# Kernel optimization log

Measured on AMD Instinct MI355X. Metric: run time of the kernel, lower is better.

Reference implementation:

```python
import jax, jax.numpy as jnp
import numpy as np

NUM_ACTIONS = 16  # number of unique leaf actions (= output_dim)


def setup_inputs() -> dict:
    key = jax.random.key(0)
    ks = jax.random.split(key, 7)
    B, IN, D, A = 32768, 128, 511, 512
    L = D + A + 1  # 1024 leaves
    x = jax.random.normal(ks[0], (B, IN), dtype=jnp.float32)
    Wd = jax.random.normal(ks[1], (D, IN), dtype=jnp.float32) * 0.05
    bd = jax.random.normal(ks[2], (D,), dtype=jnp.float32) * 0.05
    Wa = jax.random.normal(ks[3], (A, IN), dtype=jnp.float32) * 0.05
    ba = jax.random.normal(ks[4], (A,), dtype=jnp.float32) * 0.05
    Wl = jax.random.normal(ks[5], (L, 2 * (D + A)), dtype=jnp.float32) * 0.05
    seg_ids = jax.random.randint(ks[6], (L,), 0, NUM_ACTIONS, dtype=jnp.int32)
    return {"x": x, "Wd": Wd, "bd": bd, "Wa": Wa, "ba": ba, "Wl": Wl,
            "seg_ids": seg_ids}


def reference(x, Wd, bd, Wa, ba, Wl, seg_ids):
    # dual linear heads (torch Linear: y = x @ W.T + b)
    x1 = x @ Wd.T + bd            # [B, D]
    x2 = x @ Wa.T + ba            # [B, A]
    h = jnp.concatenate([x1, x2], axis=1)                     # [B, D+A]
    hh = jnp.concatenate([jax.nn.relu(h), jax.nn.relu(-h)], axis=1)  # [B, 2(D+A)]
    leaf = hh @ Wl.T              # [B, L]
    # ragged per-action max over leaf columns (MaxPoolLayer)
    pooled = jax.ops.segment_max(leaf.T, seg_ids,
                                 num_segments=NUM_ACTIONS).T   # [B, NUM_ACTIONS]
    return jax.nn.softmax(pooled, axis=-1)
```

## Files before the change

### kernel.cpp

```cpp
#include <hip/hip_runtime.h>
#include <hip/hip_bf16.h>
#include <cstdint>
#include <cmath>

#define AS1 __attribute__((address_space(1)))
#define AS3 __attribute__((address_space(3)))

typedef unsigned short u16;
typedef uint32_t u32;
typedef __attribute__((ext_vector_type(8))) __bf16 bf16x8;
typedef __attribute__((ext_vector_type(8))) unsigned short u16x8;
typedef __attribute__((ext_vector_type(4))) float f32x4;


__device__ __forceinline__ u16 f2bf(float f) {
    uint32_t u = __builtin_bit_cast(uint32_t, f);
    return (u16)((u + 0x7fffu + ((u >> 16) & 1u)) >> 16);
}

__device__ __forceinline__ u32 f2ord(float f) {
    u32 u = __builtin_bit_cast(u32, f);
    return u ^ (u32)(((int32_t)u >> 31) | 0x80000000);
}
__device__ __forceinline__ float ord2f(u32 v) {
    u32 u = (v & 0x80000000u) ? (v ^ 0x80000000u) : ~v;
    return __builtin_bit_cast(float, u);
}


__global__ void setup_all(const float* __restrict__ x,
                          const float* __restrict__ Wd, const float* __restrict__ bd,
                          const float* __restrict__ Wa, const float* __restrict__ ba,
                          const float* __restrict__ Wl,
                          u16* __restrict__ xb, u16* __restrict__ w1b,
                          float* __restrict__ bb, u16* __restrict__ w1t,
                          u16* __restrict__ wsb, u16* __restrict__ dlb,
                          float* __restrict__ cl, u32* __restrict__ pooled) {
    __shared__ float cred[256];
    const int b = blockIdx.x;
    const int tid = threadIdx.x;
    if (b < 2048) {
        long idx = (long)(b * 256 + tid) * 8;
        float4 a = *(const float4*)(x + idx);
        float4 c = *(const float4*)(x + idx + 4);
        u16x8 o;
        o[0]=f2bf(a.x); o[1]=f2bf(a.y); o[2]=f2bf(a.z); o[3]=f2bf(a.w);
        o[4]=f2bf(c.x); o[5]=f2bf(c.y); o[6]=f2bf(c.z); o[7]=f2bf(c.w);
        *(u16x8*)(xb + idx) = o;
    } else if (b < 2112) {
        int t = (b - 2048) * 256 + tid;
        int row = t >> 4, g = (t & 15) * 8;
        const float* src = nullptr;
        if (row < 511)       src = Wd + row * 128 + g;
        else if (row < 1023) src = Wa + (row - 511) * 128 + g;
        u16x8 o = 0;
        if (src) {
            #pragma unroll
            for (int j = 0; j < 8; ++j) o[j] = f2bf(src[j]);
        }
        *(u16x8*)(w1b + row * 128 + g) = o;
        #pragma unroll
        for (int j = 0; j < 8; ++j) w1t[(g + j) * 1024 + row] = o[j];
        if ((t & 15) == 0)
            bb[row] = row < 511 ? bd[row] : (row < 1023 ? ba[row - 511] : 0.f);
    } else if (b < 2624) {
        const int l0 = (b - 2112) * 2;
        const int lo = tid >> 7, g = (tid & 127) * 8;
        const float* src = Wl + (long)(l0 + lo) * 2046;
        u16x8 os, od;
        float part = 0.f;
        #pragma unroll
        for (int j = 0; j < 8; ++j) {
            int c = g + j;
            float pa = 0.f, pb = 0.f;
            if (c < 1023) { pa = src[c]; pb = src[1023 + c]; }
            os[j] = f2bf(0.5f * (pa + pb));
            float v = pa - pb;
            od[j] = f2bf(v);
            float b1 = c < 511 ? bd[c] : (c < 1023 ? ba[c - 511] : 0.f);
            part += v * b1;
        }
        *(u16x8*)(wsb + (long)(l0 + lo) * 1024 + g) = os;
        *(u16x8*)(dlb + (long)(l0 + lo) * 1024 + g) = od;
        cred[tid] = part;
        __syncthreads();
        if (tid < 2) {
            float s = 0.f;
            #pragma unroll
            for (int k = 0; k < 128; ++k) s += cred[tid * 128 + k];
            cl[l0 + tid] = 0.5f * s;
        }
    } else {
        uint4* p4 = (uint4*)pooled;
        const int base = (b - 2624) * 16384;
        #pragma unroll
        for (int j = 0; j < 64; ++j)
            p4[base + tid + j * 256] = uint4{0u, 0u, 0u, 0u};
    }
}

__global__ __launch_bounds__(256) void gemm_hwc(
        const u16* __restrict__ xb, const u16* __restrict__ w1b,
        const float* __restrict__ bb,
        const u16* __restrict__ dlb, const u16* __restrict__ w1t,
        u16* __restrict__ habs, u16* __restrict__ wcb) {
    __shared__ union SharedU {
        struct { u16 As[2][4096]; u16 Bs[2][4096]; } s;
        u16 obuf[128 * 132];
    } sh;
    const int tid  = threadIdx.x;
    const int lane = tid & 63, wave = tid >> 6;
    const int wy = wave >> 1, wx = wave & 1;
    const int i16 = lane & 15, q = lane >> 4;
    const int cA = wave * 2, srow = lane >> 2;
    const int scol = (((lane & 3) ^ ((lane >> 3) & 3))) * 8;
    const int qa   = (q ^ ((i16 >> 1) & 3)) * 8;

    f32x4 acc[4][4];
    #pragma unroll
    for (int m = 0; m < 4; ++m)
        #pragma unroll
        for (int n = 0; n < 4; ++n) acc[m][n] = f32x4{0.f,0.f,0.f,0.f};

    if (blockIdx.y == 0) {
        const long blockM = (long)blockIdx.x * 128;
        const int koff = (blockIdx.x * 4) & 31;
        const u16* a0 = dlb + (blockM + cA * 16 + srow) * 1024 + scol;
        const u16* a1 = dlb + (blockM + (cA + 1) * 16 + srow) * 1024 + scol;
        const u16* b0 = w1t + (long)(cA * 16 + srow) * 1024 + scol;
        const u16* b1 = w1t + (long)((cA + 1) * 16 + srow) * 1024 + scol;
        auto wstage = [&](int tt) {
            const int sl = tt & 1;
            const int k0 = ((tt + koff) & 31) << 5;
            __builtin_amdgcn_global_load_lds((const AS1 void*)(a0 + k0), (AS3 void*)&sh.s.As[sl][cA * 512],       16, 0, 0);
            __builtin_amdgcn_global_load_lds((const AS1 void*)(a1 + k0), (AS3 void*)&sh.s.As[sl][(cA + 1) * 512], 16, 0, 0);
            __builtin_amdgcn_global_load_lds((const AS1 void*)(b0 + k0), (AS3 void*)&sh.s.Bs[sl][cA * 512],       16, 0, 0);
            __builtin_amdgcn_global_load_lds((const AS1 void*)(b1 + k0), (AS3 void*)&sh.s.Bs[sl][(cA + 1) * 512], 16, 0, 0);
        };
        wstage(0);
        asm volatile("s_waitcnt vmcnt(0)" ::: "memory");
        __builtin_amdgcn_s_barrier();
        for (int t = 0; t < 32; ++t) {
            const int sl = t & 1;
            __builtin_amdgcn_sched_barrier(0);
            bf16x8 af[4], bfv[4];
            #pragma unroll
            for (int s = 0; s < 4; ++s) {
                af[s]  = *(const bf16x8*)&sh.s.As[sl][(wy * 64 + s * 16 + i16) * 32 + qa];
                bfv[s] = *(const bf16x8*)&sh.s.Bs[sl][(wx * 64 + s * 16 + i16) * 32 + qa];
            }
            if (t + 1 < 32) wstage(t + 1);
            asm volatile("s_waitcnt lgkmcnt(0)" ::: "memory");
            __builtin_amdgcn_sched_barrier(0);
            __builtin_amdgcn_s_setprio(1);
            #pragma unroll
            for (int sm = 0; sm < 4; ++sm)
                #pragma unroll
                for (int sn = 0; sn < 4; ++sn)
                    acc[sm][sn] = __builtin_amdgcn_mfma_f32_16x16x32_bf16(af[sm], bfv[sn], acc[sm][sn], 0, 0, 0);
            __builtin_amdgcn_s_setprio(0);
            if (t + 1 < 32) { asm volatile("s_waitcnt vmcnt(0)" ::: "memory"); }
            __builtin_amdgcn_s_barrier();
        }
        #pragma unroll
        for (int sm = 0; sm < 4; ++sm)
            #pragma unroll
            for (int sn = 0; sn < 4; ++sn) {
                const int col = wx * 64 + sn * 16 + i16;
                #pragma unroll
                for (int r = 0; r < 4; ++r) {
                    const long row = blockM + wy * 64 + sm * 16 + 4 * q + r;
                    wcb[row * 128 + col] = f2bf(0.5f * acc[sm][sn][r]);
                }
            }
        return;
    }

    const int xcd = blockIdx.x, yy = blockIdx.y - 1;
    const long blockM = (long)(xcd * 32 + (yy >> 3)) * 128;
    const int  blockN = (yy & 7) * 128;

    const u16* a0 = xb + (blockM + cA * 16 + srow) * 128 + scol;
    const u16* a1 = xb + (blockM + (cA + 1) * 16 + srow) * 128 + scol;
    const u16* b0 = w1b + ((long)blockN + cA * 16 + srow) * 128 + scol;
    const u16* b1 = w1b + ((long)blockN + (cA + 1) * 16 + srow) * 128 + scol;
    auto hstage = [&](int tt) {
        const int sl = tt & 1, kp = tt * 32;
        __builtin_amdgcn_global_load_lds((const AS1 void*)(a0 + kp), (AS3 void*)&sh.s.As[sl][cA * 512],       16, 0, 0);
        __builtin_amdgcn_global_load_lds((const AS1 void*)(a1 + kp), (AS3 void*)&sh.s.As[sl][(cA + 1) * 512], 16, 0, 0);
        __builtin_amdgcn_global_load_lds((const AS1 void*)(b0 + kp), (AS3 void*)&sh.s.Bs[sl][cA * 512],       16, 0, 0);
        __builtin_amdgcn_global_load_lds((const AS1 void*)(b1 + kp), (AS3 void*)&sh.s.Bs[sl][(cA + 1) * 512], 16, 0, 0);
    };
    hstage(0);
    asm volatile("s_waitcnt vmcnt(0)" ::: "memory");
    __builtin_amdgcn_s_barrier();
    #pragma unroll
    for (int kt = 0; kt < 4; ++kt) {
        const int sl = kt & 1;
        __builtin_amdgcn_sched_barrier(0);
        bf16x8 af[4], bfv[4];
        #pragma unroll
        for (int s = 0; s < 4; ++s) {
            af[s]  = *(const bf16x8*)&sh.s.As[sl][(wy * 64 + s * 16 + i16) * 32 + qa];
            bfv[s] = *(const bf16x8*)&sh.s.Bs[sl][(wx * 64 + s * 16 + i16) * 32 + qa];
        }
        if (kt + 1 < 4) hstage(kt + 1);
        asm volatile("s_waitcnt lgkmcnt(0)" ::: "memory");
        __builtin_amdgcn_sched_barrier(0);
        __builtin_amdgcn_s_setprio(1);
        #pragma unroll
        for (int sm = 0; sm < 4; ++sm)
            #pragma unroll
            for (int sn = 0; sn < 4; ++sn)
                acc[sm][sn] = __builtin_amdgcn_mfma_f32_16x16x32_bf16(af[sm], bfv[sn], acc[sm][sn], 0, 0, 0);
        __builtin_amdgcn_s_setprio(0);
        if (kt + 1 < 4) { asm volatile("s_waitcnt vmcnt(0)" ::: "memory"); }
        __builtin_amdgcn_s_barrier();
    }

    float bv[4];
    #pragma unroll
    for (int sn = 0; sn < 4; ++sn) bv[sn] = bb[blockN + wx * 64 + sn * 16 + i16];
    #pragma unroll
    for (int sm = 0; sm < 4; ++sm)
        #pragma unroll
        for (int sn = 0; sn < 4; ++sn)
            #pragma unroll
            for (int r = 0; r < 4; ++r)
                sh.obuf[(wy * 64 + sm * 16 + 4 * q + r) * 132 + wx * 64 + sn * 16 + i16] =
                    f2bf(fabsf(acc[sm][sn][r] + bv[sn]));
    __syncthreads();
    const int cg = (tid & 15) * 8;
    #pragma unroll
    for (int it = 0; it < 8; ++it) {
        const int row = it * 16 + (tid >> 4);
        *(u16x8*)&habs[(blockM + row) * 1024 + blockN + cg] =
            *(const u16x8*)&sh.obuf[row * 132 + cg];
    }
}

__global__ __launch_bounds__(512, 2) void gemm_leaf(const u16* __restrict__ habs,
        const u16* __restrict__ xb, const u16* __restrict__ wsb,
        const u16* __restrict__ wcb, const float* __restrict__ cl,
        const int* __restrict__ seg, u32* __restrict__ pooled) {
    __shared__ __align__(16) u16 As[4][256 * 32];
    __shared__ __align__(16) u16 Bs[4][256 * 32];
    __shared__ u32 pmax[256 * 16];
    const int tid  = threadIdx.x;
    const int lane = tid & 63, w = tid >> 6;
    const int wm = w >> 2, wn = w & 3;
    const int i16 = lane & 15, q = lane >> 4;

    const int bid  = blockIdx.x;
    const int wgid = (bid & 7) * 64 + (bid >> 3);
    const int mT = wgid >> 2, nT = wgid & 3;
    const long blockM = (long)mT * 256;
    const int  blockN = nT * 256;

    #pragma unroll
    for (int j = 0; j < 8; ++j) pmax[tid + j * 512] = 0u;

    const int r0 = tid >> 2;
    const int scol = (((tid & 3) ^ ((tid >> 3) & 3))) * 8;
    const u16* gA1 = habs + (blockM + r0) * 1024 + scol;
    const u16* gB1 = wsb  + (long)(blockN + r0) * 1024 + scol;
    const u16* gA2 = xb   + (blockM + r0) * 128 + scol;
    const u16* gB2 = wcb  + (long)(blockN + r0) * 128 + scol;
    const int ldsb = w * 512;

    auto stageA = [&](int tt) {
        u16* dst = &As[tt & 3][ldsb];
        const u16* g; int jstr;
        if (tt < 32) { g = gA1 + tt * 32;        jstr = 128 * 1024; }
        else         { g = gA2 + (tt - 32) * 32; jstr = 128 * 128; }
        __builtin_amdgcn_global_load_lds((const AS1 void*)g,          (AS3 void*)dst,          16, 0, 0);
        __builtin_amdgcn_global_load_lds((const AS1 void*)(g + jstr), (AS3 void*)(dst + 4096), 16, 0, 0);
    };
    auto stageB = [&](int tt) {
        u16* dst = &Bs[tt & 3][ldsb];
        const u16* g; int jstr;
        if (tt < 32) { g = gB1 + tt * 32;        jstr = 128 * 1024; }
        else         { g = gB2 + (tt - 32) * 32; jstr = 128 * 128; }
        __builtin_amdgcn_global_load_lds((const AS1 void*)g,          (AS3 void*)dst,          16, 0, 0);
        __builtin_amdgcn_global_load_lds((const AS1 void*)(g + jstr), (AS3 void*)(dst + 4096), 16, 0, 0);
    };

    f32x4 acc[8][4];
    #pragma unroll
    for (int m = 0; m < 8; ++m)
        #pragma unroll
        for (int n = 0; n < 4; ++n) acc[m][n] = f32x4{0.f,0.f,0.f,0.f};
    bf16x8 a0r[4], a1r[4], br[4];

    const int rdc = (q ^ ((i16 >> 1) & 3)) * 8;
    auto lda = [&](bf16x8* ar, int slot, int mh) {
        #pragma unroll
        for (int mf = 0; mf < 4; ++mf)
            ar[mf] = *(const bf16x8*)&As[slot][(wm * 128 + mh * 64 + mf * 16 + i16) * 32 + rdc];
    };
    auto ldb = [&](int slot) {
        #pragma unroll
        for (int nf = 0; nf < 4; ++nf)
            br[nf] = *(const bf16x8*)&Bs[slot][(wn * 64 + nf * 16 + i16) * 32 + rdc];
    };
    auto mf16 = [&](const bf16x8* ar, int mh) {
        #pragma unroll
        for (int mf = 0; mf < 4; ++mf)
            #pragma unroll
            for (int nf = 0; nf < 4; ++nf)
                acc[mh * 4 + mf][nf] = __builtin_amdgcn_mfma_f32_16x16x32_bf16(
                    ar[mf], br[nf], acc[mh * 4 + mf][nf], 0, 0, 0);
    };

    stageA(0); stageB(0); stageA(1); stageB(1);
    asm volatile("s_waitcnt vmcnt(4)" ::: "memory");
    __builtin_amdgcn_s_barrier();
    __builtin_amdgcn_sched_barrier(0);
    lda(a0r, 0, 0); ldb(0);

    for (int t = 0; t < 36; ++t) {
        const int slot = t & 3;
        lda(a1r, slot, 1);
        if (t + 2 < 36) { stageA(t + 2); stageB(t + 2); }
        asm volatile("s_waitcnt lgkmcnt(4)" ::: "memory");
        __builtin_amdgcn_sched_barrier(0);
        __builtin_amdgcn_s_setprio(1);
        mf16(a0r, 0);
        __builtin_amdgcn_s_setprio(0);
        asm volatile("s_waitcnt lgkmcnt(0)" ::: "memory");
        __builtin_amdgcn_sched_barrier(0);
        __builtin_amdgcn_s_setprio(1);
        mf16(a1r, 1);
        __builtin_amdgcn_s_setprio(0);
        if (t < 34)       { asm volatile("s_waitcnt vmcnt(4)" ::: "memory"); }
        else if (t == 34) { asm volatile("s_waitcnt vmcnt(0)" ::: "memory"); }
        __builtin_amdgcn_s_barrier();
        __builtin_amdgcn_sched_barrier(0);
        if (t + 1 < 36) { lda(a0r, (t + 1) & 3, 0); ldb((t + 1) & 3); }
    }

    int segc[4]; float clv[4];
    #pragma unroll
    for (int nf = 0; nf < 4; ++nf) {
        const int col = blockN + wn * 64 + nf * 16 + i16;
        segc[nf] = seg[col];
        clv[nf]  = cl[col];
    }
    #pragma unroll
    for (int mf = 0; mf < 8; ++mf)
        #pragma unroll
        for (int nf = 0; nf < 4; ++nf)
            #pragma unroll
            for (int r = 0; r < 4; ++r) {
                const int rl = wm * 128 + mf * 16 + 4 * q + r;
                atomicMax(&pmax[rl * 16 + segc[nf]], f2ord(acc[mf][nf][r] + clv[nf]));
            }
    __syncthreads();
    #pragma unroll
    for (int j = 0; j < 8; ++j) {
        int idx = tid + j * 512;
        atomicMax(&pooled[((blockM + (idx >> 4)) << 4) + (idx & 15)], pmax[idx]);
    }
}

__global__ __launch_bounds__(256) void finalize(const u32* __restrict__ pooled,
                                                float* __restrict__ out) {
    const int tid = threadIdx.x;
    const long row = (long)blockIdx.x * 16 + (tid >> 4);
    const int t = tid & 15;
    float logit = ord2f(pooled[(row << 4) + t]);
    float rm = logit;
    #pragma unroll
    for (int d = 8; d >= 1; d >>= 1) rm = fmaxf(rm, __shfl_xor(rm, d, 16));
    float e = __expf(logit - rm);
    float s = e;
    #pragma unroll
    for (int d = 8; d >= 1; d >>= 1) s += __shfl_xor(s, d, 16);
    out[(row << 4) + t] = e / s;
}

extern "C" void kernel_launch(void* const* d_in, const int* in_sizes, int n_in,
                              void* d_out, int out_size, void* d_ws, size_t ws_size,
                              hipStream_t stream) {
    const float* x  = (const float*)d_in[0];
    const float* Wd = (const float*)d_in[1];
    const float* bd = (const float*)d_in[2];
    const float* Wa = (const float*)d_in[3];
    const float* ba = (const float*)d_in[4];
    const float* Wl = (const float*)d_in[5];
    const int*  seg = (const int*)d_in[6];
    float* out = (float*)d_out;

    char* ws = (char*)d_ws;
    u16*   xb   = (u16*)(ws);
    u16*   w1b  = (u16*)(ws + 8388608);
    float* bb   = (float*)(ws + 8650752);
    u16*   w1t  = (u16*)(ws + 8654848);
    u16*   wsb  = (u16*)(ws + 8916992);
    u16*   dlb  = (u16*)(ws + 11014144);
    u16*   wcb  = (u16*)(ws + 13111296);
    float* clp  = (float*)(ws + 13373440);
    u16*   habs = (u16*)(ws + 13377536);
    u32*   pooled = (u32*)(ws + 80486400);

    setup_all<<<2632, 256, 0, stream>>>(x, Wd, bd, Wa, ba, Wl,
                                        xb, w1b, bb, w1t, wsb, dlb, clp, pooled);
    gemm_hwc <<<dim3(8, 257), 256, 0, stream>>>(xb, w1b, bb, dlb, w1t, habs, wcb);
    gemm_leaf<<<512, 512, 0, stream>>>(habs, xb, wsb, wcb, clp, seg, pooled);
    finalize <<<2048, 256, 0, stream>>>(pooled, out);
}
```

Baseline: 197.5 us.

## Shrink leaf GEMM tile to 128x256 with 4 waves and double-buffered LDS

The leaf GEMM moves from 256x256 tiles with 8 waves and a 4-stage LDS ring to 128x256 tiles with 4 waves (each wave computing 64x128) and a 2-stage buffer, launched as 1024 blocks instead of 512. The smaller per-block LDS footprint should let more blocks be resident and give finer load balancing across CUs. In exchange, B tiles are reloaded twice as often, arithmetic intensity per block is lower, and prefetch depth drops to one stage with a full vmcnt(0) wait every iteration, which exposes more memory latency.

```diff
diff --git a/kernel.cpp b/kernel.cpp
--- a/kernel.cpp
+++ b/kernel.cpp
@@ -239,26 +239,26 @@
     }
 }
 
-__global__ __launch_bounds__(512, 2) void gemm_leaf(const u16* __restrict__ habs,
+__global__ __launch_bounds__(256, 2) void gemm_leaf(const u16* __restrict__ habs,
         const u16* __restrict__ xb, const u16* __restrict__ wsb,
         const u16* __restrict__ wcb, const float* __restrict__ cl,
         const int* __restrict__ seg, u32* __restrict__ pooled) {
-    __shared__ __align__(16) u16 As[4][256 * 32];
-    __shared__ __align__(16) u16 Bs[4][256 * 32];
-    __shared__ u32 pmax[256 * 16];
+    __shared__ __align__(16) u16 As[2][128 * 32];
+    __shared__ __align__(16) u16 Bs[2][256 * 32];
+    __shared__ u32 pmax[128 * 16];
     const int tid  = threadIdx.x;
-    const int lane = tid & 63, w = tid >> 6;
-    const int wm = w >> 2, wn = w & 3;
+    const int lane = tid & 63, wave = tid >> 6;
+    const int wm = wave >> 1, wn = wave & 1;
     const int i16 = lane & 15, q = lane >> 4;
 
     const int bid  = blockIdx.x;
-    const int wgid = (bid & 7) * 64 + (bid >> 3);
+    const int wgid = (bid & 7) * 128 + (bid >> 3);
     const int mT = wgid >> 2, nT = wgid & 3;
-    const long blockM = (long)mT * 256;
+    const long blockM = (long)mT * 128;
     const int  blockN = nT * 256;
 
     #pragma unroll
-    for (int j = 0; j < 8; ++j) pmax[tid + j * 512] = 0u;
+    for (int j = 0; j < 8; ++j) pmax[tid + j * 256] = 0u;
 
     const int r0 = tid >> 2;
     const int scol = (((tid & 3) ^ ((tid >> 3) & 3))) * 8;
@@ -266,99 +266,100 @@
     const u16* gB1 = wsb  + (long)(blockN + r0) * 1024 + scol;
     const u16* gA2 = xb   + (blockM + r0) * 128 + scol;
     const u16* gB2 = wcb  + (long)(blockN + r0) * 128 + scol;
-    const int ldsb = w * 512;
+    const int ldsb = wave * 512;
 
     auto stageA = [&](int tt) {
-        u16* dst = &As[tt & 3][ldsb];
-        const u16* g; int jstr;
-        if (tt < 32) { g = gA1 + tt * 32;        jstr = 128 * 1024; }
-        else         { g = gA2 + (tt - 32) * 32; jstr = 128 * 128; }
+        u16* dst = &As[tt & 1][ldsb];
+        const u16* g; long jstr;
+        if (tt < 32) { g = gA1 + tt * 32;        jstr = 64L * 1024; }
+        else         { g = gA2 + (tt - 32) * 32; jstr = 64L * 128; }
         __builtin_amdgcn_global_load_lds((const AS1 void*)g,          (AS3 void*)dst,          16, 0, 0);
-        __builtin_amdgcn_global_load_lds((const AS1 void*)(g + jstr), (AS3 void*)(dst + 4096), 16, 0, 0);
+        __builtin_amdgcn_global_load_lds((const AS1 void*)(g + jstr), (AS3 void*)(dst + 2048), 16, 0, 0);
     };
     auto stageB = [&](int tt) {
-        u16* dst = &Bs[tt & 3][ldsb];
-        const u16* g; int jstr;
-        if (tt < 32) { g = gB1 + tt * 32;        jstr = 128 * 1024; }
-        else         { g = gB2 + (tt - 32) * 32; jstr = 128 * 128; }
-        __builtin_amdgcn_global_load_lds((const AS1 void*)g,          (AS3 void*)dst,          16, 0, 0);
-        __builtin_amdgcn_global_load_lds((const AS1 void*)(g + jstr), (AS3 void*)(dst + 4096), 16, 0, 0);
-    };
-
-    f32x4 acc[8][4];
-    #pragma unroll
-    for (int m = 0; m < 8; ++m)
-        #pragma unroll
-        for (int n = 0; n < 4; ++n) acc[m][n] = f32x4{0.f,0.f,0.f,0.f};
-    bf16x8 a0r[4], a1r[4], br[4];
+        u16* dst = &Bs[tt & 1][ldsb];
+        const u16* g; long jstr;
+        if (tt < 32) { g = gB1 + tt * 32;        jstr = 64L * 1024; }
+        else         { g = gB2 + (tt - 32) * 32; jstr = 64L * 128; }
+        #pragma unroll
+        for (int k = 0; k < 4; ++k)
+            __builtin_amdgcn_global_load_lds((const AS1 void*)(g + k * jstr),
+                                             (AS3 void*)(dst + k * 2048), 16, 0, 0);
+    };
+
+    f32x4 acc[4][8];
+    #pragma unroll
+    for (int m = 0; m < 4; ++m)
+        #pragma unroll
+        for (int n = 0; n < 8; ++n) acc[m][n] = f32x4{0.f,0.f,0.f,0.f};
+    bf16x8 a[4], b[8];
 
     const int rdc = (q ^ ((i16 >> 1) & 3)) * 8;
-    auto lda = [&](bf16x8* ar, int slot, int mh) {
+    auto lda = [&](int slot) {
         #pragma unroll
         for (int mf = 0; mf < 4; ++mf)
-            ar[mf] = *(const bf16x8*)&As[slot][(wm * 128 + mh * 64 + mf * 16 + i16) * 32 + rdc];
-    };
-    auto ldb = [&](int slot) {
+            a[mf] = *(const bf16x8*)&As[slot][(wm * 64 + mf * 16 + i16) * 32 + rdc];
+    };
+    auto ldbh = [&](int slot, int h) {
         #pragma unroll
         for (int nf = 0; nf < 4; ++nf)
-            br[nf] = *(const bf16x8*)&Bs[slot][(wn * 64 + nf * 16 + i16) * 32 + rdc];
-    };
-    auto mf16 = [&](const bf16x8* ar, int mh) {
+            b[h * 4 + nf] = *(const bf16x8*)&Bs[slot][(wn * 128 + h * 64 + nf * 16 + i16) * 32 + rdc];
+    };
+    auto mfg = [&](int h) {
         #pragma unroll
         for (int mf = 0; mf < 4; ++mf)
             #pragma unroll
             for (int nf = 0; nf < 4; ++nf)
-                acc[mh * 4 + mf][nf] = __builtin_amdgcn_mfma_f32_16x16x32_bf16(
-                    ar[mf], br[nf], acc[mh * 4 + mf][nf], 0, 0, 0);
-    };
-
-    stageA(0); stageB(0); stageA(1); stageB(1);
-    asm volatile("s_waitcnt vmcnt(4)" ::: "memory");
+                acc[mf][h * 4 + nf] = __builtin_amdgcn_mfma_f32_16x16x32_bf16(
+                    a[mf], b[h * 4 + nf], acc[mf][h * 4 + nf], 0, 0, 0);
+    };
+
+    stageA(0); stageB(0);
+    asm volatile("s_waitcnt vmcnt(0)" ::: "memory");
     __builtin_amdgcn_s_barrier();
     __builtin_amdgcn_sched_barrier(0);
-    lda(a0r, 0, 0); ldb(0);
+    lda(0); ldbh(0, 0);
 
     for (int t = 0; t < 36; ++t) {
-        const int slot = t & 3;
-        lda(a1r, slot, 1);
-        if (t + 2 < 36) { stageA(t + 2); stageB(t + 2); }
+        const int slot = t & 1;
+        ldbh(slot, 1);
+        if (t + 1 < 36) { stageA(t + 1); stageB(t + 1); }
         asm volatile("s_waitcnt lgkmcnt(4)" ::: "memory");
         __builtin_amdgcn_sched_barrier(0);
         __builtin_amdgcn_s_setprio(1);
-        mf16(a0r, 0);
+        mfg(0);
         __builtin_amdgcn_s_setprio(0);
         asm volatile("s_waitcnt lgkmcnt(0)" ::: "memory");
         __builtin_amdgcn_sched_barrier(0);
         __builtin_amdgcn_s_setprio(1);
-        mf16(a1r, 1);
+        mfg(1);
         __builtin_amdgcn_s_setprio(0);
-        if (t < 34)       { asm volatile("s_waitcnt vmcnt(4)" ::: "memory"); }
-        else if (t == 34) { asm volatile("s_waitcnt vmcnt(0)" ::: "memory"); }
+        if (t + 1 < 36) { asm volatile("s_waitcnt vmcnt(0)" ::: "memory"); }
         __builtin_amdgcn_s_barrier();
         __builtin_amdgcn_sched_barrier(0);
-        if (t + 1 < 36) { lda(a0r, (t + 1) & 3, 0); ldb((t + 1) & 3); }
-    }
-
-    int segc[4]; float clv[4];
-    #pragma unroll
-    for (int nf = 0; nf < 4; ++nf) {
-        const int col = blockN + wn * 64 + nf * 16 + i16;
+        if (t + 1 < 36) { lda((t + 1) & 1); ldbh((t + 1) & 1, 0); }
+    }
+
+    int segc[8]; float clv[8];
+    #pragma unroll
+    for (int nf = 0; nf < 8; ++nf) {
+        const int col = blockN + wn * 128 + (nf >> 2) * 64 + (nf & 3) * 16 + i16;
         segc[nf] = seg[col];
         clv[nf]  = cl[col];
     }
     #pragma unroll
-    for (int mf = 0; mf < 8; ++mf)
-        #pragma unroll
-        for (int nf = 0; nf < 4; ++nf)
+    for (int mf = 0; mf < 4; ++mf)
+        #pragma unroll
+        for (int nf = 0; nf < 8; ++nf)
             #pragma unroll
             for (int r = 0; r < 4; ++r) {
-                const int rl = wm * 128 + mf * 16 + 4 * q + r;
+                const int rl = wm * 64 + mf * 16 + 4 * q + r;
                 atomicMax(&pmax[rl * 16 + segc[nf]], f2ord(acc[mf][nf][r] + clv[nf]));
             }
     __syncthreads();
     #pragma unroll
     for (int j = 0; j < 8; ++j) {
-        int idx = tid + j * 512;
+        int idx = tid + j * 256;
         atomicMax(&pooled[((blockM + (idx >> 4)) << 4) + (idx & 15)], pmax[idx]);
     }
 }
@@ -406,6 +407,6 @@
     setup_all<<<2632, 256, 0, stream>>>(x, Wd, bd, Wa, ba, Wl,
                                         xb, w1b, bb, w1t, wsb, dlb, clp, pooled);
     gemm_hwc <<<dim3(8, 257), 256, 0, stream>>>(xb, w1b, bb, dlb, w1t, habs, wcb);
-    gemm_leaf<<<512, 512, 0, stream>>>(habs, xb, wsb, wcb, clp, seg, pooled);
+    gemm_leaf<<<1024, 256, 0, stream>>>(habs, xb, wsb, wcb, clp, seg, pooled);
     finalize <<<2048, 256, 0, stream>>>(pooled, out);
 }
```

Result: no change. 200.2 us (+1.4%).

## Load A operand directly from global into registers, drop A LDS staging

Applied to the files above, without the earlier changes.

The leaf GEMM now reads each warp's A fragments straight from global memory into registers instead of staging A tiles through LDS with async global-to-LDS loads. B keeps LDS staging but goes from four buffers to two, and the pipeline shrinks from two tiles ahead to one. This cuts LDS use and LDS traffic, which could raise occupancy. The cost is that A rows are re-read by each of the four wn warps sharing them, and the global load latency is no longer hidden because every iteration waits on vmcnt(0) before its MFMAs.

```diff
diff --git a/kernel.cpp b/kernel.cpp
--- a/kernel.cpp
+++ b/kernel.cpp
@@ -243,8 +243,7 @@
         const u16* __restrict__ xb, const u16* __restrict__ wsb,
         const u16* __restrict__ wcb, const float* __restrict__ cl,
         const int* __restrict__ seg, u32* __restrict__ pooled) {
-    __shared__ __align__(16) u16 As[4][256 * 32];
-    __shared__ __align__(16) u16 Bs[4][256 * 32];
+    __shared__ __align__(16) u16 Bs[2][256 * 32];
     __shared__ u32 pmax[256 * 16];
     const int tid  = threadIdx.x;
     const int lane = tid & 63, w = tid >> 6;
@@ -262,22 +261,12 @@
 
     const int r0 = tid >> 2;
     const int scol = (((tid & 3) ^ ((tid >> 3) & 3))) * 8;
-    const u16* gA1 = habs + (blockM + r0) * 1024 + scol;
-    const u16* gB1 = wsb  + (long)(blockN + r0) * 1024 + scol;
-    const u16* gA2 = xb   + (blockM + r0) * 128 + scol;
-    const u16* gB2 = wcb  + (long)(blockN + r0) * 128 + scol;
+    const u16* gB1 = wsb + (long)(blockN + r0) * 1024 + scol;
+    const u16* gB2 = wcb + (long)(blockN + r0) * 128 + scol;
     const int ldsb = w * 512;
 
-    auto stageA = [&](int tt) {
-        u16* dst = &As[tt & 3][ldsb];
-        const u16* g; int jstr;
-        if (tt < 32) { g = gA1 + tt * 32;        jstr = 128 * 1024; }
-        else         { g = gA2 + (tt - 32) * 32; jstr = 128 * 128; }
-        __builtin_amdgcn_global_load_lds((const AS1 void*)g,          (AS3 void*)dst,          16, 0, 0);
-        __builtin_amdgcn_global_load_lds((const AS1 void*)(g + jstr), (AS3 void*)(dst + 4096), 16, 0, 0);
-    };
     auto stageB = [&](int tt) {
-        u16* dst = &Bs[tt & 3][ldsb];
+        u16* dst = &Bs[tt & 1][ldsb];
         const u16* g; int jstr;
         if (tt < 32) { g = gB1 + tt * 32;        jstr = 128 * 1024; }
         else         { g = gB2 + (tt - 32) * 32; jstr = 128 * 128; }
@@ -285,58 +274,57 @@
         __builtin_amdgcn_global_load_lds((const AS1 void*)(g + jstr), (AS3 void*)(dst + 4096), 16, 0, 0);
     };
 
+    const u16* pAh = habs + (blockM + wm * 128 + i16) * 1024 + q * 8;
+    const u16* pAx = xb   + (blockM + wm * 128 + i16) * 128  + q * 8;
+
     f32x4 acc[8][4];
     #pragma unroll
     for (int m = 0; m < 8; ++m)
         #pragma unroll
         for (int n = 0; n < 4; ++n) acc[m][n] = f32x4{0.f,0.f,0.f,0.f};
-    bf16x8 a0r[4], a1r[4], br[4];
+    bf16x8 a[8], br[4];
 
     const int rdc = (q ^ ((i16 >> 1) & 3)) * 8;
-    auto lda = [&](bf16x8* ar, int slot, int mh) {
-        #pragma unroll
-        for (int mf = 0; mf < 4; ++mf)
-            ar[mf] = *(const bf16x8*)&As[slot][(wm * 128 + mh * 64 + mf * 16 + i16) * 32 + rdc];
+    auto ldaG = [&](int t) {
+        if (t < 32) {
+            #pragma unroll
+            for (int mf = 0; mf < 8; ++mf)
+                a[mf] = *(const bf16x8*)(pAh + mf * 16 * 1024 + t * 32);
+        } else {
+            #pragma unroll
+            for (int mf = 0; mf < 8; ++mf)
+                a[mf] = *(const bf16x8*)(pAx + mf * 16 * 128 + (t - 32) * 32);
+        }
     };
     auto ldb = [&](int slot) {
         #pragma unroll
         for (int nf = 0; nf < 4; ++nf)
             br[nf] = *(const bf16x8*)&Bs[slot][(wn * 64 + nf * 16 + i16) * 32 + rdc];
     };
-    auto mf16 = [&](const bf16x8* ar, int mh) {
-        #pragma unroll
-        for (int mf = 0; mf < 4; ++mf)
+
+    stageB(0);
+    asm volatile("s_waitcnt vmcnt(0)" ::: "memory");
+    __builtin_amdgcn_s_barrier();
+
+    for (int t = 0; t < 36; ++t) {
+        const int slot = t & 1;
+        ldaG(t);
+        ldb(slot);
+        if (t + 1 < 36) stageB(t + 1);
+        __builtin_amdgcn_s_setprio(1);
+        #pragma unroll
+        for (int mf = 0; mf < 8; ++mf)
             #pragma unroll
             for (int nf = 0; nf < 4; ++nf)
-                acc[mh * 4 + mf][nf] = __builtin_amdgcn_mfma_f32_16x16x32_bf16(
-                    ar[mf], br[nf], acc[mh * 4 + mf][nf], 0, 0, 0);
-    };
-
-    stageA(0); stageB(0); stageA(1); stageB(1);
-    asm volatile("s_waitcnt vmcnt(4)" ::: "memory");
-    __builtin_amdgcn_s_barrier();
-    __builtin_amdgcn_sched_barrier(0);
-    lda(a0r, 0, 0); ldb(0);
-
-    for (int t = 0; t < 36; ++t) {
-        const int slot = t & 3;
-        lda(a1r, slot, 1);
-        if (t + 2 < 36) { stageA(t + 2); stageB(t + 2); }
-        asm volatile("s_waitcnt lgkmcnt(4)" ::: "memory");
-        __builtin_amdgcn_sched_barrier(0);
-        __builtin_amdgcn_s_setprio(1);
-        mf16(a0r, 0);
+                acc[mf][nf] = __builtin_amdgcn_mfma_f32_16x16x32_bf16(
+                    a[mf], br[nf], acc[mf][nf], 0, 0, 0);
         __builtin_amdgcn_s_setprio(0);
-        asm volatile("s_waitcnt lgkmcnt(0)" ::: "memory");
-        __builtin_amdgcn_sched_barrier(0);
-        __builtin_amdgcn_s_setprio(1);
-        mf16(a1r, 1);
-        __builtin_amdgcn_s_setprio(0);
-        if (t < 34)       { asm volatile("s_waitcnt vmcnt(4)" ::: "memory"); }
-        else if (t == 34) { asm volatile("s_waitcnt vmcnt(0)" ::: "memory"); }
-        __builtin_amdgcn_s_barrier();
-        __builtin_amdgcn_sched_barrier(0);
-        if (t + 1 < 36) { lda(a0r, (t + 1) & 3, 0); ldb((t + 1) & 3); }
+        if (t + 1 < 36) {
+            __builtin_amdgcn_sched_barrier(0);
+            asm volatile("s_waitcnt vmcnt(0)" ::: "memory");
+            __builtin_amdgcn_s_barrier();
+            __builtin_amdgcn_sched_barrier(0);
+        }
     }
 
     int segc[4]; float clv[4];
```

After: 301.3 us. +52.6%, slower.
